# Optimization experiments

Hardware: AMD Instinct MI355X
Metric: run time of the kernel (lower is better)

The kernel has to match this reference:

```python
import jax, jax.numpy as jnp
import numpy as np

N_IN, N_OUT, H = 32, 31, 128
B1, B2 = 256, 256


def setup_inputs() -> dict:
    key = jax.random.key(0)
    ks = jax.random.split(key, 6)
    def lin(k, o, i):
        return jax.random.normal(k, (o, i), jnp.float32) / np.float32(np.sqrt(i))
    return {
        "t": jax.random.uniform(ks[0], (), jnp.float32),
        "y": jax.random.normal(ks[1], (B1, B2, N_OUT), jnp.float32),
        "W0": lin(ks[2], H, N_IN), "b0": jnp.zeros((H,), jnp.float32),
        "W1": lin(ks[3], H, H),    "b1": jnp.zeros((H,), jnp.float32),
        "W2": lin(ks[4], H, H),    "b2": jnp.zeros((H,), jnp.float32),
        "W3": lin(ks[5], N_OUT, H), "b3": jnp.zeros((N_OUT,), jnp.float32),
    }


def reference(t, y, W0, b0, W1, b1, W2, b2, W3, b3):
    # inp[..., :-1] = y ; inp[..., -1] = force(t) with force = sin
    force = jnp.sin(t)
    inp = jnp.concatenate(
        [y, jnp.broadcast_to(force, y.shape[:-1] + (1,))], axis=-1
    )  # [B1, B2, N_IN]

    def model(x):  # x: [N_IN]
        h = jnp.tanh(W0 @ x + b0)
        h = jnp.tanh(W1 @ h + b1)
        h = jnp.tanh(W2 @ h + b2)
        return W3 @ h + b3  # [N_OUT]

    out = jax.vmap(jax.vmap(model))(inp)  # [B1, B2, N_OUT]
    # vmap(vmap(jacrev(model)))(inp)[..., :-1] -> drop d/d(force) column
    jac = jax.vmap(jax.vmap(jax.jacrev(model)))(inp)[..., :-1]  # [B1,B2,N_OUT,N_IN-1]
    return out, jac
```

## Files before the change

kernel.cpp:

```cpp
#include <hip/hip_runtime.h>
#include <hip/hip_bf16.h>
#include <math.h>


using short8 = __attribute__((ext_vector_type(8))) short;
using f32x4  = __attribute__((ext_vector_type(4))) float;

#define PB 4
#define PPB 32
#define STRIDE 136

__device__ __forceinline__ float fast_tanh(float z) {
    float e = __expf(2.0f * z);
    return 1.0f - 2.0f * __builtin_amdgcn_rcpf(e + 1.0f);
}

__device__ __forceinline__ unsigned pk2(float lo, float hi) {
    unsigned r;
    asm("v_cvt_pk_bf16_f32 %0, %1, %2" : "=v"(r) : "v"(lo), "v"(hi));
    return r;
}

__device__ __forceinline__ short8 pack8f(const float* s) {
    union { unsigned u[4]; short8 v; } r;
    #pragma unroll
    for (int qq = 0; qq < 4; ++qq) r.u[qq] = pk2(s[2 * qq], s[2 * qq + 1]);
    return r.v;
}

__device__ __forceinline__ short8 load_row8(const float* p) {
    float tmp[8];
    const float4* p4 = reinterpret_cast<const float4*>(p);
    float4 q0 = p4[0], q1 = p4[1];
    tmp[0]=q0.x; tmp[1]=q0.y; tmp[2]=q0.z; tmp[3]=q0.w;
    tmp[4]=q1.x; tmp[5]=q1.y; tmp[6]=q1.z; tmp[7]=q1.w;
    return pack8f(tmp);
}

__global__ void __launch_bounds__(512, 4)
node_mfma(const float* __restrict__ tptr,
          const float* __restrict__ y,
          const float* __restrict__ W0, const float* __restrict__ b0,
          const float* __restrict__ W1, const float* __restrict__ b1,
          const float* __restrict__ W2, const float* __restrict__ b2,
          const float* __restrict__ W3, const float* __restrict__ b3,
          float* __restrict__ out, float* __restrict__ jac, int npts) {
    __shared__ __align__(16) ushort XT[2][PB][32][STRIDE];
    __shared__ __align__(16) float xb[PB][32];

    const int tid  = threadIdx.x;
    const int w    = tid >> 6;
    const int lane = tid & 63;
    const int r16  = lane & 15;
    const int g    = lane >> 4;
    const int j    = 16 * w + r16;

    short8 aW0 = load_row8(W0 + j * 32 + g * 8);
    short8 aW[2][4];
    #pragma unroll
    for (int kc = 0; kc < 4; ++kc) {
        aW[0][kc] = load_row8(W1 + j * 128 + kc * 32 + g * 8);
        aW[1][kc] = load_row8(W2 + j * 128 + kc * 32 + g * 8);
    }
    const int mw = (w >> 1) & 1, nw = w & 1;
    const int r3 = 16 * mw + r16;
    short8 aW3[4];
    #pragma unroll
    for (int kc = 0; kc < 4; ++kc) {
        if (r3 < 31) aW3[kc] = load_row8(W3 + r3 * 128 + kc * 32 + g * 8);
        else { short8 z = {0,0,0,0,0,0,0,0}; aW3[kc] = z; }
    }

    short8 oh0, oh1;
    {
        union { ushort u[8]; short8 v; } z0, z1;
        #pragma unroll
        for (int i = 0; i < 8; ++i) {
            z0.u[i] = (g == (r16 >> 3) && i == (r16 & 7)) ? (ushort)0x3F80 : (ushort)0;
            z1.u[i] = (r16 < 15 && g == ((16 + r16) >> 3) && i == ((16 + r16) & 7))
                          ? (ushort)0x3F80 : (ushort)0;
        }
        oh0 = z0.v; oh1 = z1.v;
    }

    float bv0[4], bv[2][4], b3v[4];
    #pragma unroll
    for (int reg = 0; reg < 4; ++reg) {
        bv0[reg]   = b0[16 * w + 4 * g + reg];
        bv[0][reg] = b1[16 * w + 4 * g + reg];
        bv[1][reg] = b2[16 * w + 4 * g + reg];
        int o = 16 * mw + 4 * g + reg;
        b3v[reg] = (o < 31) ? b3[o] : 0.0f;
    }
    const float force = sinf(tptr[0]);

    auto epi = [&](f32x4 a0, f32x4 a1, const float* bL4, ushort* dst) {
        float va[4], vb[4];
        #pragma unroll
        for (int reg = 0; reg < 4; ++reg) {
            float tv = fast_tanh(a1[reg] + bL4[reg]);
            float d  = 1.0f - tv * tv;
            float dd = __shfl(d, lane | 15, 64);
            va[reg] = dd * a0[reg];
            vb[reg] = (r16 == 15) ? tv : dd * a1[reg];
        }
        uint2 pa, pb;
        pa.x = pk2(va[0], va[1]); pa.y = pk2(va[2], va[3]);
        pb.x = pk2(vb[0], vb[1]); pb.y = pk2(vb[2], vb[3]);
        *reinterpret_cast<uint2*>(&dst[r16 * STRIDE + 16 * w + 4 * g])        = pa;
        *reinterpret_cast<uint2*>(&dst[(16 + r16) * STRIDE + 16 * w + 4 * g]) = pb;
    };

    const int pl0 = tid >> 5, c0 = tid & 31;
    const bool act = tid < PB * 32;
    float pf = 0.0f;
    if (act && c0 < 31) pf = y[(size_t)(blockIdx.x * PPB + pl0) * 31 + c0];

    for (int pass = 0; pass < PPB / PB; ++pass) {
        const int pbase = blockIdx.x * PPB + pass * PB;

        if (act) xb[pl0][c0] = (c0 < 31) ? pf : force;
        __syncthreads();

        #pragma unroll
        for (int pl = 0; pl < PB; ++pl) {
            float xa[8];
            const float4* xp = reinterpret_cast<const float4*>(&xb[pl][g * 8]);
            float4 x0 = xp[0], x1 = xp[1];
            xa[0]=x0.x; xa[1]=x0.y; xa[2]=x0.z; xa[3]=x0.w;
            xa[4]=x1.x; xa[5]=x1.y; xa[6]=x1.z; xa[7]=x1.w;
            short8 xpk = pack8f(xa);
            short8 bf1 = (r16 == 15) ? xpk : oh1;
            f32x4 a0 = {0.f,0.f,0.f,0.f}, a1 = {0.f,0.f,0.f,0.f};
            __builtin_amdgcn_s_setprio(1);
            a0 = __builtin_amdgcn_mfma_f32_16x16x32_bf16(aW0, oh0, a0, 0, 0, 0);
            a1 = __builtin_amdgcn_mfma_f32_16x16x32_bf16(aW0, bf1, a1, 0, 0, 0);
            __builtin_amdgcn_s_setprio(0);
            epi(a0, a1, bv0, &XT[0][pl][0][0]);
        }

        if (act && c0 < 31 && pass + 1 < PPB / PB)
            pf = y[(size_t)(pbase + PB + pl0) * 31 + c0];

        __syncthreads();

        #pragma unroll
        for (int L = 0; L < 2; ++L) {
            #pragma unroll
            for (int pl = 0; pl < PB; ++pl) {
                f32x4 a0 = {0.f, 0.f, 0.f, 0.f}, a1 = {0.f, 0.f, 0.f, 0.f};
                __builtin_amdgcn_s_setprio(1);
                #pragma unroll
                for (int kc = 0; kc < 4; ++kc) {
                    short8 bf0 = *reinterpret_cast<const short8*>(&XT[L][pl][r16][kc * 32 + g * 8]);
                    short8 bf1 = *reinterpret_cast<const short8*>(&XT[L][pl][16 + r16][kc * 32 + g * 8]);
                    a0 = __builtin_amdgcn_mfma_f32_16x16x32_bf16(aW[L][kc], bf0, a0, 0, 0, 0);
                    a1 = __builtin_amdgcn_mfma_f32_16x16x32_bf16(aW[L][kc], bf1, a1, 0, 0, 0);
                }
                __builtin_amdgcn_s_setprio(0);
                epi(a0, a1, bv[L], &XT[1 - L][pl][0][0]);
            }
            __syncthreads();
        }

        #pragma unroll
        for (int tsk = 0; tsk < 2; ++tsk) {
            int pl = (w >> 2) + tsk * 2;
            f32x4 a = {0.f, 0.f, 0.f, 0.f};
            __builtin_amdgcn_s_setprio(1);
            #pragma unroll
            for (int kc = 0; kc < 4; ++kc) {
                short8 bf = *reinterpret_cast<const short8*>(&XT[0][pl][16 * nw + r16][kc * 32 + g * 8]);
                a = __builtin_amdgcn_mfma_f32_16x16x32_bf16(aW3[kc], bf, a, 0, 0, 0);
            }
            __builtin_amdgcn_s_setprio(0);
            size_t p = (size_t)(pbase + pl);
            int c = 16 * nw + r16;
            if ((int)p < npts) {
                #pragma unroll
                for (int reg = 0; reg < 4; ++reg) {
                    int o = 16 * mw + 4 * g + reg;
                    if (o < 31) {
                        if (c == 31) out[p * 31 + o] = a[reg] + b3v[reg];
                        else         jac[(p * 31 + o) * 31 + c] = a[reg];
                    }
                }
            }
        }
    }
}

extern "C" void kernel_launch(void* const* d_in, const int* in_sizes, int n_in,
                              void* d_out, int out_size, void* d_ws, size_t ws_size,
                              hipStream_t stream) {
    const float* t  = (const float*)d_in[0];
    const float* y  = (const float*)d_in[1];
    const float* W0 = (const float*)d_in[2];
    const float* b0 = (const float*)d_in[3];
    const float* W1 = (const float*)d_in[4];
    const float* b1 = (const float*)d_in[5];
    const float* W2 = (const float*)d_in[6];
    const float* b2 = (const float*)d_in[7];
    const float* W3 = (const float*)d_in[8];
    const float* b3 = (const float*)d_in[9];

    const int npts = in_sizes[1] / 31;
    float* out = (float*)d_out;
    float* jac = out + (size_t)npts * 31;

    const int blocks = (npts + PPB - 1) / PPB;
    node_mfma<<<blocks, 512, 0, stream>>>(t, y, W0, b0, W1, b1, W2, b2, W3, b3,
                                          out, jac, npts);
}
```

Baseline: 332.1 us.

## Software-pipeline layer-3 output stage across passes to cut barriers

Restructures the per-pass schedule so that the final layer (W3 matmul and the out/jac global stores) for the previous pass runs at the start of the next pass, overlapping with layer 0 of the new pass. The two LDS buffers alternate by pass parity, and the xb staging write is moved before the last barrier, which removes one __syncthreads per pass. The y prefetch is issued earlier as well. The cost is a peeled final layer-3 call and somewhat more complex buffer-ownership logic.

```diff
diff --git a/kernel.cpp b/kernel.cpp
--- a/kernel.cpp
+++ b/kernel.cpp
@@ -8,6 +8,7 @@
 
 #define PB 4
 #define PPB 32
+#define NPASS (PPB / PB)
 #define STRIDE 136
 
 __device__ __forceinline__ float fast_tanh(float z) {
@@ -111,16 +112,49 @@
         *reinterpret_cast<uint2*>(&dst[(16 + r16) * STRIDE + 16 * w + 4 * g]) = pb;
     };
 
+    auto do_l3 = [&](int pb3, const ushort* bufb) {
+        #pragma unroll
+        for (int tsk = 0; tsk < 2; ++tsk) {
+            const int pl = (w >> 2) + tsk * 2;
+            f32x4 a = {0.f, 0.f, 0.f, 0.f};
+            __builtin_amdgcn_s_setprio(1);
+            #pragma unroll
+            for (int kc = 0; kc < 4; ++kc) {
+                short8 bf = *reinterpret_cast<const short8*>(
+                    &bufb[(pl * 32 + 16 * nw + r16) * STRIDE + kc * 32 + g * 8]);
+                a = __builtin_amdgcn_mfma_f32_16x16x32_bf16(aW3[kc], bf, a, 0, 0, 0);
+            }
+            __builtin_amdgcn_s_setprio(0);
+            const size_t p = (size_t)(pb3 + pl);
+            const int c = 16 * nw + r16;
+            if ((int)p < npts) {
+                #pragma unroll
+                for (int reg = 0; reg < 4; ++reg) {
+                    const int o = 16 * mw + 4 * g + reg;
+                    if (o < 31) {
+                        if (c == 31) out[p * 31 + o] = a[reg] + b3v[reg];
+                        else         jac[(p * 31 + o) * 31 + c] = a[reg];
+                    }
+                }
+            }
+        }
+    };
+
     const int pl0 = tid >> 5, c0 = tid & 31;
     const bool act = tid < PB * 32;
     float pf = 0.0f;
     if (act && c0 < 31) pf = y[(size_t)(blockIdx.x * PPB + pl0) * 31 + c0];
-
-    for (int pass = 0; pass < PPB / PB; ++pass) {
+    if (act) xb[pl0][c0] = (c0 < 31) ? pf : force;
+    __syncthreads();
+
+    for (int pass = 0; pass < NPASS; ++pass) {
+        const int s = pass & 1;
         const int pbase = blockIdx.x * PPB + pass * PB;
 
-        if (act) xb[pl0][c0] = (c0 < 31) ? pf : force;
-        __syncthreads();
+        if (act && c0 < 31 && pass + 1 < NPASS)
+            pf = y[(size_t)(pbase + PB + pl0) * 31 + c0];
+
+        if (pass > 0) do_l3(pbase - PB, &XT[1 - s][0][0][0]);
 
         #pragma unroll
         for (int pl = 0; pl < PB; ++pl) {
@@ -136,58 +170,45 @@
             a0 = __builtin_amdgcn_mfma_f32_16x16x32_bf16(aW0, oh0, a0, 0, 0, 0);
             a1 = __builtin_amdgcn_mfma_f32_16x16x32_bf16(aW0, bf1, a1, 0, 0, 0);
             __builtin_amdgcn_s_setprio(0);
-            epi(a0, a1, bv0, &XT[0][pl][0][0]);
-        }
-
-        if (act && c0 < 31 && pass + 1 < PPB / PB)
-            pf = y[(size_t)(pbase + PB + pl0) * 31 + c0];
-
+            epi(a0, a1, bv0, &XT[s][pl][0][0]);
+        }
         __syncthreads();
 
         #pragma unroll
-        for (int L = 0; L < 2; ++L) {
-            #pragma unroll
-            for (int pl = 0; pl < PB; ++pl) {
-                f32x4 a0 = {0.f, 0.f, 0.f, 0.f}, a1 = {0.f, 0.f, 0.f, 0.f};
-                __builtin_amdgcn_s_setprio(1);
-                #pragma unroll
-                for (int kc = 0; kc < 4; ++kc) {
-                    short8 bf0 = *reinterpret_cast<const short8*>(&XT[L][pl][r16][kc * 32 + g * 8]);
-                    short8 bf1 = *reinterpret_cast<const short8*>(&XT[L][pl][16 + r16][kc * 32 + g * 8]);
-                    a0 = __builtin_amdgcn_mfma_f32_16x16x32_bf16(aW[L][kc], bf0, a0, 0, 0, 0);
-                    a1 = __builtin_amdgcn_mfma_f32_16x16x32_bf16(aW[L][kc], bf1, a1, 0, 0, 0);
-                }
-                __builtin_amdgcn_s_setprio(0);
-                epi(a0, a1, bv[L], &XT[1 - L][pl][0][0]);
-            }
-            __syncthreads();
-        }
-
-        #pragma unroll
-        for (int tsk = 0; tsk < 2; ++tsk) {
-            int pl = (w >> 2) + tsk * 2;
-            f32x4 a = {0.f, 0.f, 0.f, 0.f};
+        for (int pl = 0; pl < PB; ++pl) {
+            f32x4 a0 = {0.f, 0.f, 0.f, 0.f}, a1 = {0.f, 0.f, 0.f, 0.f};
             __builtin_amdgcn_s_setprio(1);
             #pragma unroll
             for (int kc = 0; kc < 4; ++kc) {
-                short8 bf = *reinterpret_cast<const short8*>(&XT[0][pl][16 * nw + r16][kc * 32 + g * 8]);
-                a = __builtin_amdgcn_mfma_f32_16x16x32_bf16(aW3[kc], bf, a, 0, 0, 0);
-            }
-            __builtin_amdgcn_s_setprio(0);
-            size_t p = (size_t)(pbase + pl);
-            int c = 16 * nw + r16;
-            if ((int)p < npts) {
-                #pragma unroll
-                for (int reg = 0; reg < 4; ++reg) {
-                    int o = 16 * mw + 4 * g + reg;
-                    if (o < 31) {
-                        if (c == 31) out[p * 31 + o] = a[reg] + b3v[reg];
-                        else         jac[(p * 31 + o) * 31 + c] = a[reg];
-                    }
-                }
-            }
-        }
-    }
+                short8 bf0 = *reinterpret_cast<const short8*>(&XT[s][pl][r16][kc * 32 + g * 8]);
+                short8 bf1 = *reinterpret_cast<const short8*>(&XT[s][pl][16 + r16][kc * 32 + g * 8]);
+                a0 = __builtin_amdgcn_mfma_f32_16x16x32_bf16(aW[0][kc], bf0, a0, 0, 0, 0);
+                a1 = __builtin_amdgcn_mfma_f32_16x16x32_bf16(aW[0][kc], bf1, a1, 0, 0, 0);
+            }
+            __builtin_amdgcn_s_setprio(0);
+            epi(a0, a1, bv[0], &XT[1 - s][pl][0][0]);
+        }
+        __syncthreads();
+
+        #pragma unroll
+        for (int pl = 0; pl < PB; ++pl) {
+            f32x4 a0 = {0.f, 0.f, 0.f, 0.f}, a1 = {0.f, 0.f, 0.f, 0.f};
+            __builtin_amdgcn_s_setprio(1);
+            #pragma unroll
+            for (int kc = 0; kc < 4; ++kc) {
+                short8 bf0 = *reinterpret_cast<const short8*>(&XT[1 - s][pl][r16][kc * 32 + g * 8]);
+                short8 bf1 = *reinterpret_cast<const short8*>(&XT[1 - s][pl][16 + r16][kc * 32 + g * 8]);
+                a0 = __builtin_amdgcn_mfma_f32_16x16x32_bf16(aW[1][kc], bf0, a0, 0, 0, 0);
+                a1 = __builtin_amdgcn_mfma_f32_16x16x32_bf16(aW[1][kc], bf1, a1, 0, 0, 0);
+            }
+            __builtin_amdgcn_s_setprio(0);
+            epi(a0, a1, bv[1], &XT[s][pl][0][0]);
+        }
+        if (act && pass + 1 < NPASS) xb[pl0][c0] = (c0 < 31) ? pf : force;
+        __syncthreads();
+    }
+
+    do_l3(blockIdx.x * PPB + (NPASS - 1) * PB, &XT[(NPASS - 1) & 1][0][0][0]);
 }
 
 extern "C" void kernel_launch(void* const* d_in, const int* in_sizes, int n_in,
```

New measurement: 334.5 us. About the same (+0.7%).
